# Optimization experiments

Hardware: AMD Instinct MI355X
Metric: run time of the kernel (lower is better)

## Reference

```python
import jax, jax.numpy as jnp
import numpy as np

B, N, H, D = 1, 50000, 8, 16  # batch, nodes, heads, head_dim (hidden=128)
E = 800000                    # edges (avg degree 16)
SCALE = float(np.sqrt(D))


def setup_inputs() -> dict:
    key = jax.random.key(0)
    kq, kk, kv, ke = jax.random.split(key, 4)
    q = jax.random.normal(kq, (B, N, H, D), dtype=jnp.float32)
    k = jax.random.normal(kk, (B, N, H, D), dtype=jnp.float32)
    v = jax.random.normal(kv, (B, N, H, D), dtype=jnp.float32)
    edge_index = jax.random.randint(ke, (2, E), 0, B * N, dtype=jnp.int32)
    return {"q": q, "k": k, "v": v, "edge_index": edge_index}


def reference(q, k, v, edge_index):
    # sparse_attention_bias path with attn_bias=None (dropout not applied in this path)
    batch, n_nodes = q.shape[0], q.shape[1]
    qf = q.reshape(-1, H, D)   # [B*N, H, D]
    kf = k.reshape(-1, H, D)
    vf = v.reshape(-1, H, D)
    src_idx = edge_index[0]
    dst_idx = edge_index[1]
    src = kf[src_idx]          # [E, H, D] gather
    dest = qf[dst_idx]         # [E, H, D] gather
    # per-edge score: clamp(sum(src*dest)/scale, -5, 5) then exp
    score = jnp.exp(jnp.clip(jnp.sum(src * dest, axis=-1, keepdims=True) / SCALE, -5.0, 5.0))  # [E, H, 1]
    msg = vf[src_idx] * score  # [E, H, D]
    wV = jax.ops.segment_sum(msg, dst_idx, num_segments=batch * n_nodes)     # [B*N, H, D]
    Z = jax.ops.segment_sum(score, dst_idx, num_segments=batch * n_nodes)    # [B*N, H, 1]
    x = wV / (Z + 1e-6)
    return x.reshape(batch, n_nodes, H * D)
```

## Files before the change

### kernel.cpp

```cpp
#include <hip/hip_runtime.h>


#define HEADS 8
#define DIM 16
#define BN 64
#define CAPB 1408
#define EPB 4096
#define PBLK 1024

__device__ __forceinline__ unsigned f2bf(float f) {
    unsigned b = __float_as_uint(f);
    return (b + 0x7fffu + ((b >> 16) & 1u)) >> 16;
}
__device__ __forceinline__ float bflo(unsigned u) { return __uint_as_float(u << 16); }
__device__ __forceinline__ float bfhi(unsigned u) { return __uint_as_float(u & 0xffff0000u); }

__global__ void __launch_bounds__(PBLK) build_kernel(
        const float4* __restrict__ k4, const float4* __restrict__ v4,
        uint4* __restrict__ kv,
        const int* __restrict__ src_idx, const int* __restrict__ dst_idx,
        int* __restrict__ gcount, unsigned* __restrict__ gpart,
        int E, int NB, int pblocks, int total) {
    __shared__ int hist[800];
    __shared__ int cur[800];
    int tid = threadIdx.x;

    if ((int)blockIdx.x < pblocks) {
        for (int i = tid; i < NB; i += PBLK) hist[i] = 0;
        __syncthreads();
        int e0 = blockIdx.x * EPB + tid * 4;
        int4 d = make_int4(0, 0, 0, 0);
        bool full = (e0 + 3 < E);
        if (full) {
            d = *(const int4*)(dst_idx + e0);
            atomicAdd(&hist[d.x >> 6], 1);
            atomicAdd(&hist[d.y >> 6], 1);
            atomicAdd(&hist[d.z >> 6], 1);
            atomicAdd(&hist[d.w >> 6], 1);
        } else {
            for (int e = e0; e < E; ++e) atomicAdd(&hist[dst_idx[e] >> 6], 1);
        }
        __syncthreads();
        for (int i = tid; i < NB; i += PBLK) {
            int h = hist[i];
            int base = h ? atomicAdd(&gcount[i], h) : 0;
            cur[i] = i * CAPB + base;
        }
        __syncthreads();
        if (full) {
            int4 s = *(const int4*)(src_idx + e0);
            int bk, p;
            bk = d.x >> 6; p = atomicAdd(&cur[bk], 1);
            if (p < bk * CAPB + CAPB) gpart[p] = ((unsigned)(d.x & 63) << 26) | (unsigned)s.x;
            bk = d.y >> 6; p = atomicAdd(&cur[bk], 1);
            if (p < bk * CAPB + CAPB) gpart[p] = ((unsigned)(d.y & 63) << 26) | (unsigned)s.y;
            bk = d.z >> 6; p = atomicAdd(&cur[bk], 1);
            if (p < bk * CAPB + CAPB) gpart[p] = ((unsigned)(d.z & 63) << 26) | (unsigned)s.z;
            bk = d.w >> 6; p = atomicAdd(&cur[bk], 1);
            if (p < bk * CAPB + CAPB) gpart[p] = ((unsigned)(d.w & 63) << 26) | (unsigned)s.w;
        } else {
            for (int e = e0; e < E; ++e) {
                int dd = dst_idx[e];
                int bk = dd >> 6;
                int p = atomicAdd(&cur[bk], 1);
                if (p < bk * CAPB + CAPB)
                    gpart[p] = ((unsigned)(dd & 63) << 26) | (unsigned)src_idx[e];
            }
        }
    } else {
        int t = ((int)blockIdx.x - pblocks) * PBLK + tid;
        if (t < total) {
            int node = t >> 5;
            int seg  = t & 31;
            int isv  = seg >> 4;
            int s    = seg & 15;
            const float4* srcp = isv ? v4 : k4;
            float4 a  = srcp[(size_t)node * 32 + s * 2];
            float4 bb = srcp[(size_t)node * 32 + s * 2 + 1];
            uint4 o;
            o.x = f2bf(a.x)  | (f2bf(a.y)  << 16);
            o.y = f2bf(a.z)  | (f2bf(a.w)  << 16);
            o.z = f2bf(bb.x) | (f2bf(bb.y) << 16);
            o.w = f2bf(bb.z) | (f2bf(bb.w) << 16);
            kv[(size_t)node * 32 + isv * 16 + (s & 1) * 8 + (s >> 1)] = o;
        }
    }
}

__global__ void __launch_bounds__(PBLK) gather_kernel(
        const float4* __restrict__ q4, const uint4* __restrict__ kv,
        const int* __restrict__ gcount, const unsigned* __restrict__ gpart,
        float4* __restrict__ out4, int N) {
    __shared__ int cnt[BN];
    __shared__ int start[BN];
    __shared__ int cur[BN];
    __shared__ int list[CAPB];
    int b   = blockIdx.x;
    int tid = threadIdx.x;
    int nodeBase = b * BN;
    int nNodes = min(BN, N - nodeBase);
    int ecnt = min(gcount[b], CAPB);

    if (tid < BN) cnt[tid] = 0;
    __syncthreads();
    for (int i = tid; i < ecnt; i += PBLK)
        atomicAdd(&cnt[gpart[(size_t)b * CAPB + i] >> 26], 1);
    __syncthreads();
    if (tid < BN) start[tid] = cnt[tid];
    __syncthreads();
    for (int off = 1; off < BN; off <<= 1) {
        int t = (tid < BN && tid >= off) ? start[tid - off] : 0;
        __syncthreads();
        if (tid < BN) start[tid] += t;
        __syncthreads();
    }
    if (tid < BN) {
        int ex = start[tid] - cnt[tid];
        start[tid] = ex;
        cur[tid] = ex;
    }
    __syncthreads();
    for (int i = tid; i < ecnt; i += PBLK) {
        unsigned r = gpart[(size_t)b * CAPB + i];
        int p = atomicAdd(&cur[r >> 26], 1);
        list[p] = (int)(r & 0x03FFFFFFu);
    }
    __syncthreads();

    int w    = tid >> 6;
    int lane = tid & 63;
    int g    = lane >> 3;
    int l8   = lane & 7;

    for (int ln = w; ln < nNodes; ln += 16) {
        int cn = cnt[ln];
        int st = start[ln];
        int node = nodeBase + ln;
        size_t qbase = (size_t)node * 32 + l8 * 4;
        float4 q0 = q4[qbase + 0], q1 = q4[qbase + 1],
               q2 = q4[qbase + 2], q3 = q4[qbase + 3];
        q0.x *= 0.25f; q0.y *= 0.25f; q0.z *= 0.25f; q0.w *= 0.25f;
        q1.x *= 0.25f; q1.y *= 0.25f; q1.z *= 0.25f; q1.w *= 0.25f;
        q2.x *= 0.25f; q2.y *= 0.25f; q2.z *= 0.25f; q2.w *= 0.25f;
        q3.x *= 0.25f; q3.y *= 0.25f; q3.z *= 0.25f; q3.w *= 0.25f;

        float4 a0 = make_float4(0, 0, 0, 0), a1 = a0, a2 = a0, a3 = a0;
        float zsum = 0.f;

        for (int j = 0; j < cn; j += 8) {
            int src = list[st + min(j + g, cn - 1)];
            size_t base = (size_t)src * 32;
            uint4 ka = kv[base + l8],      kb = kv[base + 8 + l8];
            uint4 va = kv[base + 16 + l8], vb = kv[base + 24 + l8];

            float p = q0.x*bflo(ka.x) + q0.y*bfhi(ka.x) + q0.z*bflo(ka.y) + q0.w*bfhi(ka.y)
                    + q1.x*bflo(ka.z) + q1.y*bfhi(ka.z) + q1.z*bflo(ka.w) + q1.w*bfhi(ka.w)
                    + q2.x*bflo(kb.x) + q2.y*bfhi(kb.x) + q2.z*bflo(kb.y) + q2.w*bfhi(kb.y)
                    + q3.x*bflo(kb.z) + q3.y*bfhi(kb.z) + q3.z*bflo(kb.w) + q3.w*bfhi(kb.w);
            p = fminf(fmaxf(p, -5.f), 5.f);
            float s = __expf(p);
            if (j + g >= cn) s = 0.f;

            a0.x += bflo(va.x)*s; a0.y += bfhi(va.x)*s; a0.z += bflo(va.y)*s; a0.w += bfhi(va.y)*s;
            a1.x += bflo(va.z)*s; a1.y += bfhi(va.z)*s; a1.z += bflo(va.w)*s; a1.w += bfhi(va.w)*s;
            a2.x += bflo(vb.x)*s; a2.y += bfhi(vb.x)*s; a2.z += bflo(vb.y)*s; a2.w += bfhi(vb.y)*s;
            a3.x += bflo(vb.z)*s; a3.y += bfhi(vb.z)*s; a3.z += bflo(vb.w)*s; a3.w += bfhi(vb.w)*s;
            zsum += s;
        }

        #pragma unroll
        for (int off = 8; off <= 32; off <<= 1) {
            a0.x += __shfl_xor(a0.x, off, 64); a0.y += __shfl_xor(a0.y, off, 64);
            a0.z += __shfl_xor(a0.z, off, 64); a0.w += __shfl_xor(a0.w, off, 64);
            a1.x += __shfl_xor(a1.x, off, 64); a1.y += __shfl_xor(a1.y, off, 64);
            a1.z += __shfl_xor(a1.z, off, 64); a1.w += __shfl_xor(a1.w, off, 64);
            a2.x += __shfl_xor(a2.x, off, 64); a2.y += __shfl_xor(a2.y, off, 64);
            a2.z += __shfl_xor(a2.z, off, 64); a2.w += __shfl_xor(a2.w, off, 64);
            a3.x += __shfl_xor(a3.x, off, 64); a3.y += __shfl_xor(a3.y, off, 64);
            a3.z += __shfl_xor(a3.z, off, 64); a3.w += __shfl_xor(a3.w, off, 64);
            zsum += __shfl_xor(zsum, off, 64);
        }

        float inv = 1.f / (zsum + 1e-6f);
        if (g == 0) {
            out4[qbase + 0] = make_float4(a0.x*inv, a0.y*inv, a0.z*inv, a0.w*inv);
            out4[qbase + 1] = make_float4(a1.x*inv, a1.y*inv, a1.z*inv, a1.w*inv);
            out4[qbase + 2] = make_float4(a2.x*inv, a2.y*inv, a2.z*inv, a2.w*inv);
            out4[qbase + 3] = make_float4(a3.x*inv, a3.y*inv, a3.z*inv, a3.w*inv);
        }
    }
}

extern "C" void kernel_launch(void* const* d_in, const int* in_sizes, int n_in,
                              void* d_out, int out_size, void* d_ws, size_t ws_size,
                              hipStream_t stream) {
    const float* q = (const float*)d_in[0];
    const float* k = (const float*)d_in[1];
    const float* v = (const float*)d_in[2];
    const int* edge = (const int*)d_in[3];

    const int E = in_sizes[3] / 2;
    const int N = in_sizes[0] / (HEADS * DIM);
    const int NB = (N + BN - 1) / BN;
    const int pblocks = (E + EPB - 1) / EPB;
    const int total = N * 32;
    const int cblocks = (total + PBLK - 1) / PBLK;

    const int* src_idx = edge;
    const int* dst_idx = edge + E;

    int* gcount = (int*)d_ws;
    size_t gc_pad = ((size_t)NB * 4 + 255) & ~(size_t)255;
    unsigned* gpart = (unsigned*)((char*)d_ws + gc_pad);
    size_t part_end = gc_pad + (size_t)NB * CAPB * 4;
    size_t kv_off = (part_end + 255) & ~(size_t)255;
    uint4* kv = (uint4*)((char*)d_ws + kv_off);

    hipMemsetAsync(gcount, 0, (size_t)NB * sizeof(int), stream);

    build_kernel<<<pblocks + cblocks, PBLK, 0, stream>>>(
        (const float4*)k, (const float4*)v, kv, src_idx, dst_idx,
        gcount, gpart, E, NB, pblocks, total);

    gather_kernel<<<NB, PBLK, 0, stream>>>(
        (const float4*)q, kv, gcount, gpart, (float4*)d_out, N);
}
```

Before: 105.5 us.

## Split bucket regroup into separate kernel and gather with one wave per node

The former fused gather kernel sorted each bucket's edges by destination in shared memory and then looped 16 waves over 64 nodes. It is now split: a regroup kernel writes the sorted source lists back into global memory along with per-node begin and count arrays, and a new gather kernel launches one wave per node in 256-thread blocks and prefetches the next source index. The goal is to remove the tail imbalance and low occupancy of 1024-thread blocks that held a large shared list, at the cost of an extra kernel launch and an extra global write and read of the partitioned edge list.

```diff
diff --git a/kernel.cpp b/kernel.cpp
--- a/kernel.cpp
+++ b/kernel.cpp
@@ -7,6 +7,7 @@
 #define CAPB 1408
 #define EPB 4096
 #define PBLK 1024
+#define RBLK 512
 
 __device__ __forceinline__ unsigned f2bf(float f) {
     unsigned b = __float_as_uint(f);
@@ -87,10 +88,9 @@
     }
 }
 
-__global__ void __launch_bounds__(PBLK) gather_kernel(
-        const float4* __restrict__ q4, const uint4* __restrict__ kv,
-        const int* __restrict__ gcount, const unsigned* __restrict__ gpart,
-        float4* __restrict__ out4, int N) {
+__global__ void __launch_bounds__(RBLK) regroup_kernel(
+        const int* __restrict__ gcount, unsigned* __restrict__ gpart,
+        int* __restrict__ node_beg, int* __restrict__ node_cnt, int N) {
     __shared__ int cnt[BN];
     __shared__ int start[BN];
     __shared__ int cur[BN];
@@ -98,13 +98,13 @@
     int b   = blockIdx.x;
     int tid = threadIdx.x;
     int nodeBase = b * BN;
-    int nNodes = min(BN, N - nodeBase);
     int ecnt = min(gcount[b], CAPB);
+    size_t gbase = (size_t)b * CAPB;
 
     if (tid < BN) cnt[tid] = 0;
     __syncthreads();
-    for (int i = tid; i < ecnt; i += PBLK)
-        atomicAdd(&cnt[gpart[(size_t)b * CAPB + i] >> 26], 1);
+    for (int i = tid; i < ecnt; i += RBLK)
+        atomicAdd(&cnt[gpart[gbase + i] >> 26], 1);
     __syncthreads();
     if (tid < BN) start[tid] = cnt[tid];
     __syncthreads();
@@ -118,37 +118,54 @@
         int ex = start[tid] - cnt[tid];
         start[tid] = ex;
         cur[tid] = ex;
-    }
-    __syncthreads();
-    for (int i = tid; i < ecnt; i += PBLK) {
-        unsigned r = gpart[(size_t)b * CAPB + i];
+        int node = nodeBase + tid;
+        if (node < N) {
+            node_beg[node] = (int)gbase + ex;
+            node_cnt[node] = cnt[tid];
+        }
+    }
+    __syncthreads();
+    for (int i = tid; i < ecnt; i += RBLK) {
+        unsigned r = gpart[gbase + i];
         int p = atomicAdd(&cur[r >> 26], 1);
         list[p] = (int)(r & 0x03FFFFFFu);
     }
     __syncthreads();
-
-    int w    = tid >> 6;
-    int lane = tid & 63;
-    int g    = lane >> 3;
-    int l8   = lane & 7;
-
-    for (int ln = w; ln < nNodes; ln += 16) {
-        int cn = cnt[ln];
-        int st = start[ln];
-        int node = nodeBase + ln;
-        size_t qbase = (size_t)node * 32 + l8 * 4;
-        float4 q0 = q4[qbase + 0], q1 = q4[qbase + 1],
-               q2 = q4[qbase + 2], q3 = q4[qbase + 3];
-        q0.x *= 0.25f; q0.y *= 0.25f; q0.z *= 0.25f; q0.w *= 0.25f;
-        q1.x *= 0.25f; q1.y *= 0.25f; q1.z *= 0.25f; q1.w *= 0.25f;
-        q2.x *= 0.25f; q2.y *= 0.25f; q2.z *= 0.25f; q2.w *= 0.25f;
-        q3.x *= 0.25f; q3.y *= 0.25f; q3.z *= 0.25f; q3.w *= 0.25f;
-
-        float4 a0 = make_float4(0, 0, 0, 0), a1 = a0, a2 = a0, a3 = a0;
-        float zsum = 0.f;
-
-        for (int j = 0; j < cn; j += 8) {
-            int src = list[st + min(j + g, cn - 1)];
+    for (int i = tid; i < ecnt; i += RBLK)
+        gpart[gbase + i] = (unsigned)list[i];
+}
+
+__global__ void gather_kernel(const float4* __restrict__ q4,
+                              const uint4* __restrict__ kv,
+                              const int* __restrict__ node_beg,
+                              const int* __restrict__ node_cnt,
+                              const unsigned* __restrict__ gpart,
+                              float4* __restrict__ out4, int n) {
+    int wave = (blockIdx.x * blockDim.x + threadIdx.x) >> 6;
+    if (wave >= n) return;
+    int lane = threadIdx.x & 63;
+    int g  = lane >> 3;
+    int l8 = lane & 7;
+
+    size_t qbase = (size_t)wave * 32 + l8 * 4;
+    float4 q0 = q4[qbase + 0], q1 = q4[qbase + 1], q2 = q4[qbase + 2], q3 = q4[qbase + 3];
+    q0.x *= 0.25f; q0.y *= 0.25f; q0.z *= 0.25f; q0.w *= 0.25f;
+    q1.x *= 0.25f; q1.y *= 0.25f; q1.z *= 0.25f; q1.w *= 0.25f;
+    q2.x *= 0.25f; q2.y *= 0.25f; q2.z *= 0.25f; q2.w *= 0.25f;
+    q3.x *= 0.25f; q3.y *= 0.25f; q3.z *= 0.25f; q3.w *= 0.25f;
+
+    float4 a0 = make_float4(0,0,0,0), a1 = a0, a2 = a0, a3 = a0;
+    float zsum = 0.f;
+    int cnt = node_cnt[wave];
+    int beg = node_beg[wave];
+
+    if (cnt > 0) {
+        const unsigned* __restrict__ row = gpart + beg;
+        int src_cur = (int)row[min(g, cnt - 1)];
+        for (int j = 0; j < cnt; j += 8) {
+            int src = src_cur;
+            src_cur = (int)row[min(j + 8 + g, cnt - 1)];
+
             size_t base = (size_t)src * 32;
             uint4 ka = kv[base + l8],      kb = kv[base + 8 + l8];
             uint4 va = kv[base + 16 + l8], vb = kv[base + 24 + l8];
@@ -159,7 +176,7 @@
                     + q3.x*bflo(kb.z) + q3.y*bfhi(kb.z) + q3.z*bflo(kb.w) + q3.w*bfhi(kb.w);
             p = fminf(fmaxf(p, -5.f), 5.f);
             float s = __expf(p);
-            if (j + g >= cn) s = 0.f;
+            if (j + g >= cnt) s = 0.f;
 
             a0.x += bflo(va.x)*s; a0.y += bfhi(va.x)*s; a0.z += bflo(va.y)*s; a0.w += bfhi(va.y)*s;
             a1.x += bflo(va.z)*s; a1.y += bfhi(va.z)*s; a1.z += bflo(va.w)*s; a1.w += bfhi(va.w)*s;
@@ -167,27 +184,27 @@
             a3.x += bflo(vb.z)*s; a3.y += bfhi(vb.z)*s; a3.z += bflo(vb.w)*s; a3.w += bfhi(vb.w)*s;
             zsum += s;
         }
-
-        #pragma unroll
-        for (int off = 8; off <= 32; off <<= 1) {
-            a0.x += __shfl_xor(a0.x, off, 64); a0.y += __shfl_xor(a0.y, off, 64);
-            a0.z += __shfl_xor(a0.z, off, 64); a0.w += __shfl_xor(a0.w, off, 64);
-            a1.x += __shfl_xor(a1.x, off, 64); a1.y += __shfl_xor(a1.y, off, 64);
-            a1.z += __shfl_xor(a1.z, off, 64); a1.w += __shfl_xor(a1.w, off, 64);
-            a2.x += __shfl_xor(a2.x, off, 64); a2.y += __shfl_xor(a2.y, off, 64);
-            a2.z += __shfl_xor(a2.z, off, 64); a2.w += __shfl_xor(a2.w, off, 64);
-            a3.x += __shfl_xor(a3.x, off, 64); a3.y += __shfl_xor(a3.y, off, 64);
-            a3.z += __shfl_xor(a3.z, off, 64); a3.w += __shfl_xor(a3.w, off, 64);
-            zsum += __shfl_xor(zsum, off, 64);
-        }
-
-        float inv = 1.f / (zsum + 1e-6f);
-        if (g == 0) {
-            out4[qbase + 0] = make_float4(a0.x*inv, a0.y*inv, a0.z*inv, a0.w*inv);
-            out4[qbase + 1] = make_float4(a1.x*inv, a1.y*inv, a1.z*inv, a1.w*inv);
-            out4[qbase + 2] = make_float4(a2.x*inv, a2.y*inv, a2.z*inv, a2.w*inv);
-            out4[qbase + 3] = make_float4(a3.x*inv, a3.y*inv, a3.z*inv, a3.w*inv);
-        }
+    }
+
+    #pragma unroll
+    for (int off = 8; off <= 32; off <<= 1) {
+        a0.x += __shfl_xor(a0.x, off, 64); a0.y += __shfl_xor(a0.y, off, 64);
+        a0.z += __shfl_xor(a0.z, off, 64); a0.w += __shfl_xor(a0.w, off, 64);
+        a1.x += __shfl_xor(a1.x, off, 64); a1.y += __shfl_xor(a1.y, off, 64);
+        a1.z += __shfl_xor(a1.z, off, 64); a1.w += __shfl_xor(a1.w, off, 64);
+        a2.x += __shfl_xor(a2.x, off, 64); a2.y += __shfl_xor(a2.y, off, 64);
+        a2.z += __shfl_xor(a2.z, off, 64); a2.w += __shfl_xor(a2.w, off, 64);
+        a3.x += __shfl_xor(a3.x, off, 64); a3.y += __shfl_xor(a3.y, off, 64);
+        a3.z += __shfl_xor(a3.z, off, 64); a3.w += __shfl_xor(a3.w, off, 64);
+        zsum += __shfl_xor(zsum, off, 64);
+    }
+
+    float inv = 1.f / (zsum + 1e-6f);
+    if (g == 0) {
+        out4[qbase + 0] = make_float4(a0.x*inv, a0.y*inv, a0.z*inv, a0.w*inv);
+        out4[qbase + 1] = make_float4(a1.x*inv, a1.y*inv, a1.z*inv, a1.w*inv);
+        out4[qbase + 2] = make_float4(a2.x*inv, a2.y*inv, a2.z*inv, a2.w*inv);
+        out4[qbase + 3] = make_float4(a3.x*inv, a3.y*inv, a3.z*inv, a3.w*inv);
     }
 }
 
@@ -213,7 +230,10 @@
     size_t gc_pad = ((size_t)NB * 4 + 255) & ~(size_t)255;
     unsigned* gpart = (unsigned*)((char*)d_ws + gc_pad);
     size_t part_end = gc_pad + (size_t)NB * CAPB * 4;
-    size_t kv_off = (part_end + 255) & ~(size_t)255;
+    int* node_beg = (int*)((char*)d_ws + part_end);
+    int* node_cnt = node_beg + N;
+    size_t meta_end = part_end + (size_t)2 * N * 4;
+    size_t kv_off = (meta_end + 255) & ~(size_t)255;
     uint4* kv = (uint4*)((char*)d_ws + kv_off);
 
     hipMemsetAsync(gcount, 0, (size_t)NB * sizeof(int), stream);
@@ -222,6 +242,13 @@
         (const float4*)k, (const float4*)v, kv, src_idx, dst_idx,
         gcount, gpart, E, NB, pblocks, total);
 
-    gather_kernel<<<NB, PBLK, 0, stream>>>(
-        (const float4*)q, kv, gcount, gpart, (float4*)d_out, N);
-}
+    regroup_kernel<<<NB, RBLK, 0, stream>>>(gcount, gpart, node_beg, node_cnt, N);
+
+    {
+        long long threads = (long long)N * 64;
+        int block = 256;
+        int grid = (int)((threads + block - 1) / block);
+        gather_kernel<<<grid, block, 0, stream>>>(
+            (const float4*)q, kv, node_beg, node_cnt, gpart, (float4*)d_out, N);
+    }
+}
```

After: 96.88 us. 1.09x faster.
